# Optimization experiments

Measured on AMD Instinct MI355X. Metric: run time of the kernel, lower is better.

Reference implementation:

```python
import jax, jax.numpy as jnp
import numpy as np


def setup_inputs() -> dict:
    key = jax.random.key(0)
    k1, k2 = jax.random.split(key)
    B, Tq, Tk, D = 16, 1024, 1024, 1024
    decoder_hidden = jax.random.normal(k1, (B, Tq, D), dtype=jnp.float32)
    encoder_outputs = jax.random.normal(k2, (B, Tk, D), dtype=jnp.float32)
    return {"decoder_hidden": decoder_hidden, "encoder_outputs": encoder_outputs}


def reference(decoder_hidden, encoder_outputs):
    # Unscaled Luong dot-product attention: bmm -> softmax -> bmm
    # scores: [B, Tq, Tk]
    scores = jnp.einsum("bqd,bkd->bqk", decoder_hidden, encoder_outputs)
    weights = jax.nn.softmax(scores, axis=-1)
    # context: [B, Tq, D]
    return jnp.einsum("bqk,bkd->bqd", weights, encoder_outputs)
```

## Files before the change

kernel.cpp:

```cpp
#include <hip/hip_runtime.h>
#include <hip/hip_fp16.h>
#include <stdint.h>


typedef _Float16 half_t;
typedef __attribute__((ext_vector_type(8))) _Float16 f16x8;
typedef __attribute__((ext_vector_type(2))) _Float16 f16x2;
typedef __attribute__((ext_vector_type(4))) float f32x4;

__global__ __launch_bounds__(256) void cvt_kernel(
    const float* __restrict__ enc,
    half_t* __restrict__ encsw, half_t* __restrict__ encTsw) {
    __shared__ half_t lt[64 * 65];
    const int b = blockIdx.z;
    const int rt = blockIdx.x, ct = blockIdx.y;
    const int t = threadIdx.x;
    const int r = t >> 2;
    const int c0 = (t & 3) << 4;
    const size_t bofs = (size_t)b << 20;

    const float* src = enc + bofs + (size_t)(rt * 64 + r) * 1024 + ct * 64 + c0;
    const float4* s4 = (const float4*)src;
    const float4 f0 = s4[0];
    const float4 f1 = s4[1];
    const float4 f2 = s4[2];
    const float4 f3 = s4[3];

    union { half_t h[16]; uint4 q[2]; } v;
    v.h[0]  = (half_t)f0.x; v.h[1]  = (half_t)f0.y;
    v.h[2]  = (half_t)f0.z; v.h[3]  = (half_t)f0.w;
    v.h[4]  = (half_t)f1.x; v.h[5]  = (half_t)f1.y;
    v.h[6]  = (half_t)f1.z; v.h[7]  = (half_t)f1.w;
    v.h[8]  = (half_t)f2.x; v.h[9]  = (half_t)f2.y;
    v.h[10] = (half_t)f2.z; v.h[11] = (half_t)f2.w;
    v.h[12] = (half_t)f3.x; v.h[13] = (half_t)f3.y;
    v.h[14] = (half_t)f3.z; v.h[15] = (half_t)f3.w;

    {
        const int gr = rt * 64 + r, gc = ct * 64 + c0;
        half_t* dst = encsw + bofs
                      + (size_t)(gc >> 5) * 32768 + gr * 32 + (gc & 31);
        ((uint4*)dst)[0] = v.q[0];
        ((uint4*)dst)[1] = v.q[1];
    }

#pragma unroll
    for (int i = 0; i < 16; ++i) lt[r * 65 + c0 + i] = v.h[i];
    __syncthreads();
    union { half_t h[16]; uint4 q[2]; } w;
#pragma unroll
    for (int i = 0; i < 16; ++i) w.h[i] = lt[(c0 + i) * 65 + r];
    const int gk = rt * 64 + c0, gd = ct * 64 + r;
    half_t* dstT = encTsw + bofs
                   + (size_t)(gk >> 5) * 32768 + gd * 32 + (gk & 31);
    ((uint4*)dstT)[0] = w.q[0];
    ((uint4*)dstT)[1] = w.q[1];
}

__global__ __launch_bounds__(512, 2) void fused_kernel(
    const float* __restrict__ dec, const half_t* __restrict__ encsw,
    const half_t* __restrict__ encTsw, float* __restrict__ out) {
    __shared__ __align__(16) unsigned char smem[65536];
    half_t* qlds = (half_t*)smem;
    half_t* plds = (half_t*)smem;
    float* red = (float*)smem;
    float* redg = (float*)(smem + 2048);

    const int l = blockIdx.x;
    const int xcd = l & 7, idx = l >> 3;
    const int b = xcd + ((idx >> 4) << 3);
    const int qbase = (idx & 15) * 64;

    const int tid = threadIdx.x;
    const int w = tid >> 6, lane = tid & 63, quad = lane >> 4, n16 = lane & 15;
    const int laneoff = n16 * 32 + quad * 8;
    const size_t bofs = (size_t)b << 20;

    const int sr = tid >> 3;
    const int sp = tid & 7;
    const int sg = (sr >> 1) & 3;
    const float* srcrow = dec + bofs + (size_t)(qbase + sr) * 1024;

    int aoff[4];
#pragma unroll
    for (int rb = 0; rb < 4; ++rb) {
        const int lr = rb * 16 + n16;
        aoff[rb] = lr * 32 + ((quad ^ ((lr >> 1) & 3)) << 3);
    }

    f32x4 acc[4][8];
#pragma unroll
    for (int rb = 0; rb < 4; ++rb)
#pragma unroll
        for (int cf = 0; cf < 8; ++cf) acc[rb][cf] = (f32x4){0.f, 0.f, 0.f, 0.f};

#pragma unroll
    for (int ph = 0; ph < 2; ++ph) {
        if (ph) __syncthreads();
#pragma unroll
        for (int k = 0; k < 4; ++k) {
            const int c0 = sp * 16 + k * 128;
            const float4* spv = (const float4*)(srcrow + ph * 512 + c0);
            const float4 a0 = spv[0], a1 = spv[1], a2 = spv[2], a3 = spv[3];
            union { half_t h[16]; uint4 q[2]; } u;
            u.h[0]  = (half_t)a0.x; u.h[1]  = (half_t)a0.y;
            u.h[2]  = (half_t)a0.z; u.h[3]  = (half_t)a0.w;
            u.h[4]  = (half_t)a1.x; u.h[5]  = (half_t)a1.y;
            u.h[6]  = (half_t)a1.z; u.h[7]  = (half_t)a1.w;
            u.h[8]  = (half_t)a2.x; u.h[9]  = (half_t)a2.y;
            u.h[10] = (half_t)a2.z; u.h[11] = (half_t)a2.w;
            u.h[12] = (half_t)a3.x; u.h[13] = (half_t)a3.y;
            u.h[14] = (half_t)a3.z; u.h[15] = (half_t)a3.w;
            const int chunk = c0 >> 5;
            const int s0 = (c0 & 31) >> 3;
            half_t* base = qlds + chunk * 2048 + sr * 32;
            ((uint4*)(base + ((s0 ^ sg) << 3)))[0] = u.q[0];
            ((uint4*)(base + (((s0 + 1) ^ sg) << 3)))[0] = u.q[1];
        }
        __syncthreads();

        for (int dcl = 0; dcl < 16; ++dcl) {
            const int dc = ph * 16 + dcl;
            const half_t* ec = encsw + bofs + (size_t)dc * 32768;
            f16x8 bf[8];
#pragma unroll
            for (int h = 0; h < 2; ++h)
#pragma unroll
                for (int cb = 0; cb < 4; ++cb)
                    bf[h * 4 + cb] = *(const f16x8*)(
                        ec + (h * 512 + w * 64 + cb * 16) * 32 + laneoff);
            f16x8 af[4];
#pragma unroll
            for (int rb = 0; rb < 4; ++rb)
                af[rb] = *(const f16x8*)(qlds + dcl * 2048 + aoff[rb]);
#pragma unroll
            for (int rb = 0; rb < 4; ++rb)
#pragma unroll
                for (int cf = 0; cf < 8; ++cf)
                    acc[rb][cf] = __builtin_amdgcn_mfma_f32_16x16x32_f16(
                        af[rb], bf[cf], acc[rb][cf], 0, 0, 0);
        }
    }
    __syncthreads();

    float mrow[4][4], srow[4][4];
#pragma unroll
    for (int rb = 0; rb < 4; ++rb)
#pragma unroll
        for (int r = 0; r < 4; ++r) {
            float m = -1e30f;
#pragma unroll
            for (int cf = 0; cf < 8; ++cf) m = fmaxf(m, acc[rb][cf][r]);
#pragma unroll
            for (int off = 1; off < 16; off <<= 1)
                m = fmaxf(m, __shfl_xor(m, off, 64));
            mrow[rb][r] = m;
        }
    if (n16 == 0) {
#pragma unroll
        for (int rb = 0; rb < 4; ++rb)
#pragma unroll
            for (int r = 0; r < 4; ++r)
                red[w * 64 + rb * 16 + quad * 4 + r] = mrow[rb][r];
    }
    __syncthreads();
    if (tid < 64) {
        float g = red[tid];
#pragma unroll
        for (int ww = 1; ww < 8; ++ww) g = fmaxf(g, red[ww * 64 + tid]);
        redg[tid] = g;
    }
    __syncthreads();
#pragma unroll
    for (int rb = 0; rb < 4; ++rb)
#pragma unroll
        for (int r = 0; r < 4; ++r) mrow[rb][r] = redg[rb * 16 + quad * 4 + r];
    __syncthreads();

#pragma unroll
    for (int rb = 0; rb < 4; ++rb)
#pragma unroll
        for (int r = 0; r < 4; ++r) {
            float s = 0.f;
#pragma unroll
            for (int cf = 0; cf < 8; ++cf) {
                float p = __expf(acc[rb][cf][r] - mrow[rb][r]);
                acc[rb][cf][r] = p;
                s += p;
            }
#pragma unroll
            for (int off = 1; off < 16; off <<= 1) s += __shfl_xor(s, off, 64);
            srow[rb][r] = s;
        }
    if (n16 == 0) {
#pragma unroll
        for (int rb = 0; rb < 4; ++rb)
#pragma unroll
            for (int r = 0; r < 4; ++r)
                red[w * 64 + rb * 16 + quad * 4 + r] = srow[rb][r];
    }
    __syncthreads();
    if (tid < 64) {
        float g = 0.f;
#pragma unroll
        for (int ww = 0; ww < 8; ++ww) g += red[ww * 64 + tid];
        redg[tid] = g;
    }
    __syncthreads();
#pragma unroll
    for (int rb = 0; rb < 4; ++rb)
#pragma unroll
        for (int r = 0; r < 4; ++r)
            srow[rb][r] = 1.0f / redg[rb * 16 + quad * 4 + r];

    f16x2 hp[4][4][2];
#pragma unroll
    for (int rb = 0; rb < 4; ++rb)
#pragma unroll
        for (int cb = 0; cb < 4; ++cb)
#pragma unroll
            for (int pr = 0; pr < 2; ++pr) {
                f16x2 t;
                t[0] = (half_t)(acc[rb][4 + cb][2 * pr] * srow[rb][2 * pr]);
                t[1] = (half_t)(acc[rb][4 + cb][2 * pr + 1] * srow[rb][2 * pr + 1]);
                hp[rb][cb][pr] = t;
            }
    __syncthreads();

#pragma unroll
    for (int rb = 0; rb < 4; ++rb)
#pragma unroll
        for (int cb = 0; cb < 4; ++cb) {
            const int cl = w * 64 + cb * 16 + n16;
            const int chunk = cl >> 5;
            const int l8 = (cl & 31) >> 3;
            const int c7 = cl & 7;
#pragma unroll
            for (int r = 0; r < 4; ++r) {
                const int lr = rb * 16 + quad * 4 + r;
                const int g = (lr >> 1) & 3;
                plds[chunk * 2048 + lr * 32 + (((l8 ^ g)) << 3) + c7] =
                    (half_t)(acc[rb][cb][r] * srow[rb][r]);
            }
        }
    __syncthreads();

    f32x4 accv[4][8];
#pragma unroll
    for (int rb = 0; rb < 4; ++rb)
#pragma unroll
        for (int cb = 0; cb < 8; ++cb) accv[rb][cb] = (f32x4){0.f, 0.f, 0.f, 0.f};

    for (int kcl = 0; kcl < 16; ++kcl) {
        const half_t* tc = encTsw + bofs + (size_t)kcl * 32768;
        f16x8 bf[8];
#pragma unroll
        for (int cb = 0; cb < 8; ++cb)
            bf[cb] = *(const f16x8*)(tc + (w * 128 + cb * 16) * 32 + laneoff);
        f16x8 af[4];
#pragma unroll
        for (int rb = 0; rb < 4; ++rb)
            af[rb] = *(const f16x8*)(plds + kcl * 2048 + aoff[rb]);
#pragma unroll
        for (int rb = 0; rb < 4; ++rb)
#pragma unroll
            for (int cb = 0; cb < 8; ++cb)
                accv[rb][cb] = __builtin_amdgcn_mfma_f32_16x16x32_f16(
                    af[rb], bf[cb], accv[rb][cb], 0, 0, 0);
    }
    __syncthreads();

#pragma unroll
    for (int rb = 0; rb < 4; ++rb)
#pragma unroll
        for (int cb = 0; cb < 4; ++cb) {
            const int cl = w * 64 + cb * 16 + n16;
            const int chunk = cl >> 5;
            const int l8 = (cl & 31) >> 3;
            const int c7 = cl & 7;
#pragma unroll
            for (int r = 0; r < 4; ++r) {
                const int lr = rb * 16 + quad * 4 + r;
                const int g = (lr >> 1) & 3;
                plds[chunk * 2048 + lr * 32 + (((l8 ^ g)) << 3) + c7] =
                    hp[rb][cb][r >> 1][r & 1];
            }
        }
    __syncthreads();

    for (int kcl = 0; kcl < 16; ++kcl) {
        const half_t* tc = encTsw + bofs + (size_t)(16 + kcl) * 32768;
        f16x8 bf[8];
#pragma unroll
        for (int cb = 0; cb < 8; ++cb)
            bf[cb] = *(const f16x8*)(tc + (w * 128 + cb * 16) * 32 + laneoff);
        f16x8 af[4];
#pragma unroll
        for (int rb = 0; rb < 4; ++rb)
            af[rb] = *(const f16x8*)(plds + kcl * 2048 + aoff[rb]);
#pragma unroll
        for (int rb = 0; rb < 4; ++rb)
#pragma unroll
            for (int cb = 0; cb < 8; ++cb)
                accv[rb][cb] = __builtin_amdgcn_mfma_f32_16x16x32_f16(
                    af[rb], bf[cb], accv[rb][cb], 0, 0, 0);
    }

#pragma unroll
    for (int rb = 0; rb < 4; ++rb)
#pragma unroll
        for (int cb = 0; cb < 8; ++cb)
#pragma unroll
            for (int r = 0; r < 4; ++r) {
                const int row = qbase + rb * 16 + quad * 4 + r;
                const int col = w * 128 + cb * 16 + n16;
                out[bofs + (size_t)row * 1024 + col] = accv[rb][cb][r];
            }
}

extern "C" void kernel_launch(void* const* d_in, const int* in_sizes, int n_in,
                              void* d_out, int out_size, void* d_ws, size_t ws_size,
                              hipStream_t stream) {
    (void)in_sizes; (void)n_in; (void)out_size; (void)ws_size;
    const float* dec = (const float*)d_in[0];
    const float* enc = (const float*)d_in[1];
    float* out = (float*)d_out;

    half_t* encsw  = (half_t*)d_ws;
    half_t* encTsw = encsw + ((size_t)16 << 20);

    cvt_kernel<<<dim3(16, 16, 16), 256, 0, stream>>>(enc, encsw, encTsw);
    fused_kernel<<<dim3(256), 512, 0, stream>>>(dec, encsw, encTsw, out);
}
```

Baseline: 278.9 us.

## Software-pipeline global B-fragment loads and rotate chunk order per block

The B operand fragments read from global memory are now register-double-buffered: each iteration issues the next chunk's loads right after the MFMAs that consume the current fragment, and the first fragment of each GEMM phase is prefetched early. Each block also starts its K-chunk loop at a rotated offset, so blocks sharing a batch touch different parts of the encoder tensor at the same moment. This is meant to hide global/L2 latency behind MFMA work and spread cache traffic, at the cost of more live registers under a launch bound of two blocks per CU.

```diff
diff --git a/kernel.cpp b/kernel.cpp
--- a/kernel.cpp
+++ b/kernel.cpp
@@ -70,6 +70,7 @@
     const int xcd = l & 7, idx = l >> 3;
     const int b = xcd + ((idx >> 4) << 3);
     const int qbase = (idx & 15) * 64;
+    const int rot = idx & 31;
 
     const int tid = threadIdx.x;
     const int w = tid >> 6, lane = tid & 63, quad = lane >> 4, n16 = lane & 15;
@@ -93,6 +94,15 @@
     for (int rb = 0; rb < 4; ++rb)
 #pragma unroll
         for (int cf = 0; cf < 8; ++cf) acc[rb][cf] = (f32x4){0.f, 0.f, 0.f, 0.f};
+
+    f16x8 bf[8];
+    {
+        const half_t* ec = encsw + bofs + (size_t)(rot & 15) * 32768;
+#pragma unroll
+        for (int cb = 0; cb < 8; ++cb)
+            bf[cb] = *(const f16x8*)(
+                ec + ((cb >> 2) * 512 + w * 64 + (cb & 3) * 16) * 32 + laneoff);
+    }
 
 #pragma unroll
     for (int ph = 0; ph < 2; ++ph) {
@@ -120,25 +130,24 @@
         __syncthreads();
 
         for (int dcl = 0; dcl < 16; ++dcl) {
-            const int dc = ph * 16 + dcl;
-            const half_t* ec = encsw + bofs + (size_t)dc * 32768;
-            f16x8 bf[8];
-#pragma unroll
-            for (int h = 0; h < 2; ++h)
-#pragma unroll
-                for (int cb = 0; cb < 4; ++cb)
-                    bf[h * 4 + cb] = *(const f16x8*)(
-                        ec + (h * 512 + w * 64 + cb * 16) * 32 + laneoff);
+            const int j = (dcl + rot) & 15;
+            const int jn = (dcl + 1 + rot) & 15;
+            const int dcn = (dcl < 15) ? (ph * 16 + jn)
+                                       : (ph == 0 ? 16 + (rot & 15) : 16 + j);
+            const half_t* ecn = encsw + bofs + (size_t)dcn * 32768;
             f16x8 af[4];
 #pragma unroll
             for (int rb = 0; rb < 4; ++rb)
-                af[rb] = *(const f16x8*)(qlds + dcl * 2048 + aoff[rb]);
-#pragma unroll
-            for (int rb = 0; rb < 4; ++rb)
-#pragma unroll
-                for (int cf = 0; cf < 8; ++cf)
-                    acc[rb][cf] = __builtin_amdgcn_mfma_f32_16x16x32_f16(
-                        af[rb], bf[cf], acc[rb][cf], 0, 0, 0);
+                af[rb] = *(const f16x8*)(qlds + j * 2048 + aoff[rb]);
+#pragma unroll
+            for (int cb = 0; cb < 8; ++cb) {
+#pragma unroll
+                for (int rb = 0; rb < 4; ++rb)
+                    acc[rb][cb] = __builtin_amdgcn_mfma_f32_16x16x32_f16(
+                        af[rb], bf[cb], acc[rb][cb], 0, 0, 0);
+                bf[cb] = *(const f16x8*)(
+                    ecn + ((cb >> 2) * 512 + w * 64 + (cb & 3) * 16) * 32 + laneoff);
+            }
         }
     }
     __syncthreads();
@@ -225,6 +234,13 @@
                 t[1] = (half_t)(acc[rb][4 + cb][2 * pr + 1] * srow[rb][2 * pr + 1]);
                 hp[rb][cb][pr] = t;
             }
+
+    {
+        const half_t* tc = encTsw + bofs + (size_t)(rot & 15) * 32768;
+#pragma unroll
+        for (int cb = 0; cb < 8; ++cb)
+            bf[cb] = *(const f16x8*)(tc + (w * 128 + cb * 16) * 32 + laneoff);
+    }
     __syncthreads();
 
 #pragma unroll
@@ -252,21 +268,22 @@
         for (int cb = 0; cb < 8; ++cb) accv[rb][cb] = (f32x4){0.f, 0.f, 0.f, 0.f};
 
     for (int kcl = 0; kcl < 16; ++kcl) {
-        const half_t* tc = encTsw + bofs + (size_t)kcl * 32768;
-        f16x8 bf[8];
-#pragma unroll
-        for (int cb = 0; cb < 8; ++cb)
-            bf[cb] = *(const f16x8*)(tc + (w * 128 + cb * 16) * 32 + laneoff);
+        const int j = (kcl + rot) & 15;
+        const int jn = (kcl + 1 + rot) & 15;
+        const int kcn = (kcl < 15) ? jn : (16 + (rot & 15));
+        const half_t* tcn = encTsw + bofs + (size_t)kcn * 32768;
         f16x8 af[4];
 #pragma unroll
         for (int rb = 0; rb < 4; ++rb)
-            af[rb] = *(const f16x8*)(plds + kcl * 2048 + aoff[rb]);
-#pragma unroll
-        for (int rb = 0; rb < 4; ++rb)
-#pragma unroll
-            for (int cb = 0; cb < 8; ++cb)
+            af[rb] = *(const f16x8*)(plds + j * 2048 + aoff[rb]);
+#pragma unroll
+        for (int cb = 0; cb < 8; ++cb) {
+#pragma unroll
+            for (int rb = 0; rb < 4; ++rb)
                 accv[rb][cb] = __builtin_amdgcn_mfma_f32_16x16x32_f16(
                     af[rb], bf[cb], accv[rb][cb], 0, 0, 0);
+            bf[cb] = *(const f16x8*)(tcn + (w * 128 + cb * 16) * 32 + laneoff);
+        }
     }
     __syncthreads();
 
@@ -289,21 +306,22 @@
     __syncthreads();
 
     for (int kcl = 0; kcl < 16; ++kcl) {
-        const half_t* tc = encTsw + bofs + (size_t)(16 + kcl) * 32768;
-        f16x8 bf[8];
-#pragma unroll
-        for (int cb = 0; cb < 8; ++cb)
-            bf[cb] = *(const f16x8*)(tc + (w * 128 + cb * 16) * 32 + laneoff);
+        const int j = (kcl + rot) & 15;
+        const int jn = (kcl + 1 + rot) & 15;
+        const int kcn = (kcl < 15) ? (16 + jn) : (16 + j);
+        const half_t* tcn = encTsw + bofs + (size_t)kcn * 32768;
         f16x8 af[4];
 #pragma unroll
         for (int rb = 0; rb < 4; ++rb)
-            af[rb] = *(const f16x8*)(plds + kcl * 2048 + aoff[rb]);
-#pragma unroll
-        for (int rb = 0; rb < 4; ++rb)
-#pragma unroll
-            for (int cb = 0; cb < 8; ++cb)
+            af[rb] = *(const f16x8*)(plds + j * 2048 + aoff[rb]);
+#pragma unroll
+        for (int cb = 0; cb < 8; ++cb) {
+#pragma unroll
+            for (int rb = 0; rb < 4; ++rb)
                 accv[rb][cb] = __builtin_amdgcn_mfma_f32_16x16x32_f16(
                     af[rb], bf[cb], accv[rb][cb], 0, 0, 0);
+            bf[cb] = *(const f16x8*)(tcn + (w * 128 + cb * 16) * 32 + laneoff);
+        }
     }
 
 #pragma unroll
```

Measured after the change: 287.5 us. 1.03x slower.
